# Performance work log

Measured on AMD Instinct MI355X. Metric: run time of the kernel, lower is better.

## Reference

```python
import jax, jax.numpy as jnp
import numpy as np

UNITS = 1024

def setup_inputs() -> dict:
    key = jax.random.key(0)
    k1, k2, k3 = jax.random.split(key, 3)
    B, T, F = 128, 256, 4
    sequence = jax.random.normal(k1, (B, T, F), dtype=jnp.float32)
    # small init scale keeps the ReLU cell state from exploding over 256 steps
    W = jax.random.normal(k2, (F, 4 * UNITS), dtype=jnp.float32) * 0.05
    U = jax.random.normal(k3, (UNITS, 4 * UNITS), dtype=jnp.float32) * 0.02
    b = jnp.zeros((4 * UNITS,), dtype=jnp.float32)
    return {"sequence": sequence, "W": W, "U": U, "b": b}

def _lstm_relu(sequence, W, U, b):
    B = sequence.shape[0]
    h0 = jnp.zeros((B, UNITS), dtype=sequence.dtype)
    c0 = jnp.zeros((B, UNITS), dtype=sequence.dtype)
    # precompute input projections for all timesteps: [T, B, 4H]
    x_proj = jnp.einsum('btf,fg->tbg', sequence, W) + b

    def step(carry, xp_t):
        h, c = carry
        z = xp_t + h @ U  # [B, 4H], gate order i,f,c,o (Keras)
        zi, zf, zg, zo = jnp.split(z, 4, axis=-1)
        i = jax.nn.sigmoid(zi)
        f = jax.nn.sigmoid(zf)
        g = jax.nn.relu(zg)          # activation=relu for candidate
        o = jax.nn.sigmoid(zo)
        c_new = f * c + i * g
        h_new = o * jax.nn.relu(c_new)  # activation=relu on cell output
        return (h_new, c_new), h_new

    (h_last, c_last), outs = jax.lax.scan(step, (h0, c0), x_proj)
    output = jnp.transpose(outs, (1, 0, 2))  # [B, T, H]
    return output, h_last, c_last

def reference(sequence, W, U, b):
    return _lstm_relu(sequence, W, U, b)
```

## Files before the change

### kernel.cpp

```cpp
#include <hip/hip_runtime.h>
#include <hip/hip_bf16.h>
#include <cstdint>


#define B_SZ   128
#define T_SZ   256
#define H_SZ   1024
#define G_SZ   4096

typedef __attribute__((ext_vector_type(8))) short short8;
typedef __attribute__((ext_vector_type(4))) float f32x4;

__device__ __forceinline__ short f2bf(float f) {
    union { float f; unsigned u; } a; a.f = f;
    unsigned r = a.u + 0x7fffu + ((a.u >> 16) & 1u);
    return (short)(r >> 16);
}

__device__ __forceinline__ float sigmoidf_(float x) {
    return 1.0f / (1.0f + __expf(-x));
}

__device__ __forceinline__ short8 pack8(f32x4 a, f32x4 b) {
    union { f32x4 v; unsigned u[4]; } ua, ub; ua.v = a; ub.v = b;
    union { short8 s; unsigned d[4]; } r;
    r.d[0] = __builtin_amdgcn_perm(ua.u[1] + 0x8000u, ua.u[0] + 0x8000u, 0x07060302u);
    r.d[1] = __builtin_amdgcn_perm(ua.u[3] + 0x8000u, ua.u[2] + 0x8000u, 0x07060302u);
    r.d[2] = __builtin_amdgcn_perm(ub.u[1] + 0x8000u, ub.u[0] + 0x8000u, 0x07060302u);
    r.d[3] = __builtin_amdgcn_perm(ub.u[3] + 0x8000u, ub.u[2] + 0x8000u, 0x07060302u);
    return r.s;
}

template<int BF16EX>
__global__ __launch_bounds__(256, 1)
void lstm_persistent(const float* __restrict__ x, const float* __restrict__ W,
                     const float* __restrict__ U, const float* __restrict__ bias,
                     float* __restrict__ out, unsigned* __restrict__ flags,
                     short* __restrict__ ex)
{
    __shared__ __align__(16) char smem[65536];
    short* Ust = (short*)smem;
    float* zpA = (float*)smem;
    float* zpB = (float*)(smem + 32768);

    const int tid  = threadIdx.x;
    const int bid  = blockIdx.x;
    const int rb   = bid >> 6;
    const int jb   = bid & 63;
    const int w    = tid >> 6;
    const int lane = tid & 63;
    const int q    = lane >> 4;
    const int n    = lane & 15;

    short8 bfrag[8][4];
    for (int kc = 0; kc < 4; ++kc) {
        const int kbase = kc * 256;
        for (int i = tid; i < 256 * 64; i += 256) {
            int k = i >> 6, col = i & 63;
            int gcol = (col >> 4) * 1024 + jb * 16 + (col & 15);
            Ust[k * 64 + col] = f2bf(U[(size_t)(kbase + k) * G_SZ + gcol]);
        }
        __syncthreads();
        if (w == kc) {
            #pragma unroll
            for (int kk = 0; kk < 8; ++kk) {
                #pragma unroll
                for (int g = 0; g < 4; ++g) {
                    short8 bb;
                    #pragma unroll
                    for (int jj = 0; jj < 8; ++jj)
                        bb[jj] = Ust[(kk * 32 + q * 8 + jj) * 64 + g * 16 + n];
                    bfrag[kk][g] = bb;
                }
            }
        }
        __syncthreads();
    }

    const int row_l  = tid >> 4;
    const int hid_l  = tid & 15;
    const int hid_g  = jb * 16 + hid_l;
    const int row_g0 = rb * 32 + row_l;
    const int row_g1 = row_g0 + 16;
    const int qr = row_l >> 2, vr = row_l & 3;
    float Wr[4][4], br[4];
    #pragma unroll
    for (int g = 0; g < 4; ++g) {
        br[g] = bias[g * 1024 + hid_g];
        #pragma unroll
        for (int f = 0; f < 4; ++f)
            Wr[g][f] = W[(size_t)f * G_SZ + g * 1024 + hid_g];
    }
    float c0 = 0.f, c1 = 0.f;

    const int arow0 = rb * 32 + n;
    const int krow  = w * 256 + q * 8;
    const unsigned* pollp = flags + rb * 256 + w * 64 + lane;
    unsigned* pubp = flags + rb * 256 + jb * 4 + w;

    for (int t = 0; t < T_SZ; ++t) {
        f32x4 xv0 = *(const f32x4*)(x + ((size_t)row_g0 * T_SZ + t) * 4);
        f32x4 xv1 = *(const f32x4*)(x + ((size_t)row_g1 * T_SZ + t) * 4);

        short8 af[8][2];
        if (t == 0) {
            short8 z = {};
            #pragma unroll
            for (int kk = 0; kk < 8; ++kk) { af[kk][0] = z; af[kk][1] = z; }
        } else {
            for (;;) {
                unsigned v = __hip_atomic_load(pollp, __ATOMIC_RELAXED,
                                               __HIP_MEMORY_SCOPE_AGENT);
                if (__all((int)(v >= (unsigned)t))) break;
                __builtin_amdgcn_s_sleep(2);
            }
            __atomic_signal_fence(__ATOMIC_ACQUIRE);

            if (BF16EX) {
                #pragma unroll
                for (int kk = 0; kk < 8; ++kk) {
                    #pragma unroll
                    for (int mt = 0; mt < 2; ++mt) {
                        const short* p = ex +
                            ((size_t)(arow0 + mt * 16) * T_SZ + (t - 1)) * H_SZ +
                            krow + kk * 32;
                        af[kk][mt] = *(const short8*)p;
                    }
                }
            } else {
                #pragma unroll
                for (int kk = 0; kk < 8; ++kk) {
                    #pragma unroll
                    for (int mt = 0; mt < 2; ++mt) {
                        const float* p = out +
                            ((size_t)(arow0 + mt * 16) * T_SZ + (t - 1)) * H_SZ +
                            krow + kk * 32;
                        f32x4 lo = *(const f32x4*)p;
                        f32x4 hi = *(const f32x4*)(p + 4);
                        af[kk][mt] = pack8(lo, hi);
                    }
                }
            }
        }

        f32x4 acc[2][4];
        #pragma unroll
        for (int mt = 0; mt < 2; ++mt)
            #pragma unroll
            for (int g = 0; g < 4; ++g)
                acc[mt][g] = (f32x4){0.f, 0.f, 0.f, 0.f};

        #pragma unroll
        for (int kk = 0; kk < 8; ++kk)
            #pragma unroll
            for (int mt = 0; mt < 2; ++mt)
                #pragma unroll
                for (int g = 0; g < 4; ++g)
                    acc[mt][g] = __builtin_amdgcn_mfma_f32_16x16x32_bf16(
                        af[kk][mt], bfrag[kk][g], acc[mt][g], 0, 0, 0);

        float* zp = (t & 1) ? zpB : zpA;
        #pragma unroll
        for (int mt = 0; mt < 2; ++mt)
            #pragma unroll
            for (int g = 0; g < 4; ++g)
                *(f32x4*)&zp[(((w * 2 + mt) * 4 + g) * 4 + q) * 64 + n * 4] =
                    acc[mt][g];
        __syncthreads();

        float hn0, hn1;
        {
            float z[4];
            #pragma unroll
            for (int g = 0; g < 4; ++g) {
                float s = br[g];
                #pragma unroll
                for (int ww = 0; ww < 4; ++ww)
                    s += zp[(((ww * 2 + 0) * 4 + g) * 4 + qr) * 64 + hid_l * 4 + vr];
                s += xv0[0] * Wr[g][0] + xv0[1] * Wr[g][1] +
                     xv0[2] * Wr[g][2] + xv0[3] * Wr[g][3];
                z[g] = s;
            }
            float ig = sigmoidf_(z[0]), fg = sigmoidf_(z[1]);
            float gg = fmaxf(z[2], 0.f), og = sigmoidf_(z[3]);
            c0 = fg * c0 + ig * gg;
            hn0 = og * fmaxf(c0, 0.f);
        }
        {
            float z[4];
            #pragma unroll
            for (int g = 0; g < 4; ++g) {
                float s = br[g];
                #pragma unroll
                for (int ww = 0; ww < 4; ++ww)
                    s += zp[(((ww * 2 + 1) * 4 + g) * 4 + qr) * 64 + hid_l * 4 + vr];
                s += xv1[0] * Wr[g][0] + xv1[1] * Wr[g][1] +
                     xv1[2] * Wr[g][2] + xv1[3] * Wr[g][3];
                z[g] = s;
            }
            float ig = sigmoidf_(z[0]), fg = sigmoidf_(z[1]);
            float gg = fmaxf(z[2], 0.f), og = sigmoidf_(z[3]);
            c1 = fg * c1 + ig * gg;
            hn1 = og * fmaxf(c1, 0.f);
        }

        if (BF16EX) {
            float o0 = __shfl_down(hn0, 1);
            float o1 = __shfl_down(hn1, 1);
            if ((hid_l & 1) == 0) {
                unsigned w0 = (unsigned)(unsigned short)f2bf(hn0) |
                              ((unsigned)(unsigned short)f2bf(o0) << 16);
                unsigned w1 = (unsigned)(unsigned short)f2bf(hn1) |
                              ((unsigned)(unsigned short)f2bf(o1) << 16);
                __hip_atomic_store(
                    (unsigned*)&ex[((size_t)row_g0 * T_SZ + t) * H_SZ + hid_g],
                    w0, __ATOMIC_RELAXED, __HIP_MEMORY_SCOPE_AGENT);
                __hip_atomic_store(
                    (unsigned*)&ex[((size_t)row_g1 * T_SZ + t) * H_SZ + hid_g],
                    w1, __ATOMIC_RELAXED, __HIP_MEMORY_SCOPE_AGENT);
            }
            out[((size_t)row_g0 * T_SZ + t) * H_SZ + hid_g] = hn0;
            out[((size_t)row_g1 * T_SZ + t) * H_SZ + hid_g] = hn1;
        } else {
            __hip_atomic_store((unsigned*)&out[((size_t)row_g0 * T_SZ + t) * H_SZ + hid_g],
                               __float_as_uint(hn0), __ATOMIC_RELAXED,
                               __HIP_MEMORY_SCOPE_AGENT);
            __hip_atomic_store((unsigned*)&out[((size_t)row_g1 * T_SZ + t) * H_SZ + hid_g],
                               __float_as_uint(hn1), __ATOMIC_RELAXED,
                               __HIP_MEMORY_SCOPE_AGENT);
        }

        if (t == T_SZ - 1) {
            float* hlast = out + (size_t)B_SZ * T_SZ * H_SZ;
            float* clast = hlast + (size_t)B_SZ * H_SZ;
            hlast[(size_t)row_g0 * H_SZ + hid_g] = hn0;
            hlast[(size_t)row_g1 * H_SZ + hid_g] = hn1;
            clast[(size_t)row_g0 * H_SZ + hid_g] = c0;
            clast[(size_t)row_g1 * H_SZ + hid_g] = c1;
        } else {
            asm volatile("s_waitcnt vmcnt(0)" ::: "memory");
            if (lane == 0)
                __hip_atomic_store(pubp, (unsigned)(t + 1),
                                   __ATOMIC_RELAXED, __HIP_MEMORY_SCOPE_AGENT);
        }
    }
}

extern "C" void kernel_launch(void* const* d_in, const int* in_sizes, int n_in,
                              void* d_out, int out_size, void* d_ws, size_t ws_size,
                              hipStream_t stream) {
    const float* x    = (const float*)d_in[0];
    const float* W    = (const float*)d_in[1];
    const float* U    = (const float*)d_in[2];
    const float* bias = (const float*)d_in[3];
    float* out = (float*)d_out;

    unsigned* flags = (unsigned*)d_ws;
    short* ex = (short*)((char*)d_ws + 4096);

    hipMemsetAsync(d_ws, 0, 4096, stream);

    const size_t need = 4096 + (size_t)B_SZ * T_SZ * H_SZ * sizeof(short);
    if (ws_size >= need) {
        hipLaunchKernelGGL((lstm_persistent<1>), dim3(256), dim3(256), 0, stream,
                           x, W, U, bias, out, flags, ex);
    } else {
        hipLaunchKernelGGL((lstm_persistent<0>), dim3(256), dim3(256), 0, stream,
                           x, W, U, bias, out, flags, ex);
    }
}
```

Baseline: 1.645 ms.

## Retile persistent LSTM blocks to 16 rows by 32 hidden units

Reassigns each persistent block from 32 batch rows × 16 hidden units to 16 batch rows × 32 hidden units. Each block now holds twice the U fragments in registers, and each sync group shrinks from 64 to 32 producers per row cluster. Padded LDS strides are added to reduce bank conflicts. The fp32 output store is moved after the flag publish so the BF16 exchange no longer waits on it. The cost is higher register pressure from 64 B fragments and a different polling pattern, which could spill or lower clocks.

```diff
diff --git a/kernel.cpp b/kernel.cpp
--- a/kernel.cpp
+++ b/kernel.cpp
@@ -7,9 +7,12 @@
 #define T_SZ   256
 #define H_SZ   1024
 #define G_SZ   4096
+#define ULD    130
+#define ZLD    68
 
 typedef __attribute__((ext_vector_type(8))) short short8;
 typedef __attribute__((ext_vector_type(4))) float f32x4;
+typedef __attribute__((ext_vector_type(2))) float f32x2;
 
 __device__ __forceinline__ short f2bf(float f) {
     union { float f; unsigned u; } a; a.f = f;
@@ -38,75 +41,78 @@
                      float* __restrict__ out, unsigned* __restrict__ flags,
                      short* __restrict__ ex)
 {
-    __shared__ __align__(16) char smem[65536];
+    __shared__ __align__(16) char smem[69632];
     short* Ust = (short*)smem;
     float* zpA = (float*)smem;
-    float* zpB = (float*)(smem + 32768);
+    float* zpB = (float*)(smem + 34816);
 
     const int tid  = threadIdx.x;
     const int bid  = blockIdx.x;
-    const int rb   = bid >> 6;
-    const int jb   = bid & 63;
+    const int cl   = bid & 7;
+    const int jbb  = bid >> 3;
     const int w    = tid >> 6;
     const int lane = tid & 63;
     const int q    = lane >> 4;
     const int n    = lane & 15;
 
-    short8 bfrag[8][4];
+    short8 bfrag[8][8];
     for (int kc = 0; kc < 4; ++kc) {
         const int kbase = kc * 256;
-        for (int i = tid; i < 256 * 64; i += 256) {
-            int k = i >> 6, col = i & 63;
-            int gcol = (col >> 4) * 1024 + jb * 16 + (col & 15);
-            Ust[k * 64 + col] = f2bf(U[(size_t)(kbase + k) * G_SZ + gcol]);
+        for (int i = tid; i < 256 * 128; i += 256) {
+            int k = i >> 7, col = i & 127;
+            int g = col >> 5, rem = col & 31;
+            Ust[k * ULD + col] =
+                f2bf(U[(size_t)(kbase + k) * G_SZ + g * 1024 + jbb * 32 + rem]);
         }
         __syncthreads();
         if (w == kc) {
             #pragma unroll
             for (int kk = 0; kk < 8; ++kk) {
                 #pragma unroll
-                for (int g = 0; g < 4; ++g) {
+                for (int tile = 0; tile < 8; ++tile) {
                     short8 bb;
                     #pragma unroll
                     for (int jj = 0; jj < 8; ++jj)
-                        bb[jj] = Ust[(kk * 32 + q * 8 + jj) * 64 + g * 16 + n];
-                    bfrag[kk][g] = bb;
+                        bb[jj] = Ust[(kk * 32 + q * 8 + jj) * ULD + tile * 16 + n];
+                    bfrag[kk][tile] = bb;
                 }
             }
         }
         __syncthreads();
     }
 
-    const int row_l  = tid >> 4;
-    const int hid_l  = tid & 15;
-    const int hid_g  = jb * 16 + hid_l;
-    const int row_g0 = rb * 32 + row_l;
-    const int row_g1 = row_g0 + 16;
-    const int qr = row_l >> 2, vr = row_l & 3;
-    float Wr[4][4], br[4];
+    const int r_l   = tid >> 4;
+    const int cp    = tid & 15;
+    const int row_g = cl * 16 + r_l;
+    const int u0    = jbb * 32 + cp * 2;
+    const int hf    = cp >> 3;
+    const int c0    = (cp * 2) & 15;
+    const int qr    = r_l >> 2, vr = r_l & 3;
+    float Wr[2][4][4], br[2][4];
     #pragma unroll
-    for (int g = 0; g < 4; ++g) {
-        br[g] = bias[g * 1024 + hid_g];
-        #pragma unroll
-        for (int f = 0; f < 4; ++f)
-            Wr[g][f] = W[(size_t)f * G_SZ + g * 1024 + hid_g];
-    }
-    float c0 = 0.f, c1 = 0.f;
-
-    const int arow0 = rb * 32 + n;
-    const int krow  = w * 256 + q * 8;
-    const unsigned* pollp = flags + rb * 256 + w * 64 + lane;
-    unsigned* pubp = flags + rb * 256 + jb * 4 + w;
+    for (int j = 0; j < 2; ++j)
+        #pragma unroll
+        for (int g = 0; g < 4; ++g) {
+            br[j][g] = bias[g * 1024 + u0 + j];
+            #pragma unroll
+            for (int f = 0; f < 4; ++f)
+                Wr[j][g][f] = W[(size_t)f * G_SZ + g * 1024 + u0 + j];
+        }
+    float cst[2] = {0.f, 0.f};
+
+    const int arow = cl * 16 + n;
+    const int krow = w * 256 + q * 8;
+    const unsigned* pollp = flags + cl * 128 + w * 32 + (lane & 31);
+    unsigned* pubp = flags + cl * 128 + jbb * 4 + w;
 
     for (int t = 0; t < T_SZ; ++t) {
-        f32x4 xv0 = *(const f32x4*)(x + ((size_t)row_g0 * T_SZ + t) * 4);
-        f32x4 xv1 = *(const f32x4*)(x + ((size_t)row_g1 * T_SZ + t) * 4);
-
-        short8 af[8][2];
+        f32x4 xv = *(const f32x4*)(x + ((size_t)row_g * T_SZ + t) * 4);
+
+        short8 af[8];
         if (t == 0) {
             short8 z = {};
             #pragma unroll
-            for (int kk = 0; kk < 8; ++kk) { af[kk][0] = z; af[kk][1] = z; }
+            for (int kk = 0; kk < 8; ++kk) af[kk] = z;
         } else {
             for (;;) {
                 unsigned v = __hip_atomic_load(pollp, __ATOMIC_RELAXED,
@@ -118,130 +124,88 @@
 
             if (BF16EX) {
                 #pragma unroll
+                for (int kk = 0; kk < 8; ++kk)
+                    af[kk] = *(const short8*)(ex +
+                        ((size_t)arow * T_SZ + (t - 1)) * H_SZ + krow + kk * 32);
+            } else {
+                #pragma unroll
                 for (int kk = 0; kk < 8; ++kk) {
-                    #pragma unroll
-                    for (int mt = 0; mt < 2; ++mt) {
-                        const short* p = ex +
-                            ((size_t)(arow0 + mt * 16) * T_SZ + (t - 1)) * H_SZ +
-                            krow + kk * 32;
-                        af[kk][mt] = *(const short8*)p;
-                    }
+                    const float* p = out +
+                        ((size_t)arow * T_SZ + (t - 1)) * H_SZ + krow + kk * 32;
+                    f32x4 lo = *(const f32x4*)p;
+                    f32x4 hi = *(const f32x4*)(p + 4);
+                    af[kk] = pack8(lo, hi);
                 }
-            } else {
-                #pragma unroll
-                for (int kk = 0; kk < 8; ++kk) {
-                    #pragma unroll
-                    for (int mt = 0; mt < 2; ++mt) {
-                        const float* p = out +
-                            ((size_t)(arow0 + mt * 16) * T_SZ + (t - 1)) * H_SZ +
-                            krow + kk * 32;
-                        f32x4 lo = *(const f32x4*)p;
-                        f32x4 hi = *(const f32x4*)(p + 4);
-                        af[kk][mt] = pack8(lo, hi);
-                    }
-                }
-            }
-        }
-
-        f32x4 acc[2][4];
-        #pragma unroll
-        for (int mt = 0; mt < 2; ++mt)
-            #pragma unroll
-            for (int g = 0; g < 4; ++g)
-                acc[mt][g] = (f32x4){0.f, 0.f, 0.f, 0.f};
+            }
+        }
+
+        f32x4 acc[8];
+        #pragma unroll
+        for (int tl = 0; tl < 8; ++tl) acc[tl] = (f32x4){0.f, 0.f, 0.f, 0.f};
 
         #pragma unroll
         for (int kk = 0; kk < 8; ++kk)
             #pragma unroll
-            for (int mt = 0; mt < 2; ++mt)
-                #pragma unroll
-                for (int g = 0; g < 4; ++g)
-                    acc[mt][g] = __builtin_amdgcn_mfma_f32_16x16x32_bf16(
-                        af[kk][mt], bfrag[kk][g], acc[mt][g], 0, 0, 0);
+            for (int tl = 0; tl < 8; ++tl)
+                acc[tl] = __builtin_amdgcn_mfma_f32_16x16x32_bf16(
+                    af[kk], bfrag[kk][tl], acc[tl], 0, 0, 0);
 
         float* zp = (t & 1) ? zpB : zpA;
         #pragma unroll
-        for (int mt = 0; mt < 2; ++mt)
-            #pragma unroll
-            for (int g = 0; g < 4; ++g)
-                *(f32x4*)&zp[(((w * 2 + mt) * 4 + g) * 4 + q) * 64 + n * 4] =
-                    acc[mt][g];
+        for (int tl = 0; tl < 8; ++tl)
+            *(f32x4*)&zp[(size_t)(((w * 8 + tl) * 4 + q) * ZLD) + n * 4] = acc[tl];
         __syncthreads();
 
-        float hn0, hn1;
-        {
+        float hh[2];
+        #pragma unroll
+        for (int j = 0; j < 2; ++j) {
             float z[4];
             #pragma unroll
             for (int g = 0; g < 4; ++g) {
-                float s = br[g];
+                float s = br[j][g];
                 #pragma unroll
                 for (int ww = 0; ww < 4; ++ww)
-                    s += zp[(((ww * 2 + 0) * 4 + g) * 4 + qr) * 64 + hid_l * 4 + vr];
-                s += xv0[0] * Wr[g][0] + xv0[1] * Wr[g][1] +
-                     xv0[2] * Wr[g][2] + xv0[3] * Wr[g][3];
+                    s += zp[(size_t)(((ww * 8 + g * 2 + hf) * 4 + qr) * ZLD) +
+                            (c0 + j) * 4 + vr];
+                s += xv[0] * Wr[j][g][0] + xv[1] * Wr[j][g][1] +
+                     xv[2] * Wr[j][g][2] + xv[3] * Wr[j][g][3];
                 z[g] = s;
             }
             float ig = sigmoidf_(z[0]), fg = sigmoidf_(z[1]);
             float gg = fmaxf(z[2], 0.f), og = sigmoidf_(z[3]);
-            c0 = fg * c0 + ig * gg;
-            hn0 = og * fmaxf(c0, 0.f);
-        }
-        {
-            float z[4];
-            #pragma unroll
-            for (int g = 0; g < 4; ++g) {
-                float s = br[g];
-                #pragma unroll
-                for (int ww = 0; ww < 4; ++ww)
-                    s += zp[(((ww * 2 + 1) * 4 + g) * 4 + qr) * 64 + hid_l * 4 + vr];
-                s += xv1[0] * Wr[g][0] + xv1[1] * Wr[g][1] +
-                     xv1[2] * Wr[g][2] + xv1[3] * Wr[g][3];
-                z[g] = s;
-            }
-            float ig = sigmoidf_(z[0]), fg = sigmoidf_(z[1]);
-            float gg = fmaxf(z[2], 0.f), og = sigmoidf_(z[3]);
-            c1 = fg * c1 + ig * gg;
-            hn1 = og * fmaxf(c1, 0.f);
-        }
-
+            cst[j] = fg * cst[j] + ig * gg;
+            hh[j] = og * fmaxf(cst[j], 0.f);
+        }
+
+        const size_t obase = ((size_t)row_g * T_SZ + t) * H_SZ + u0;
         if (BF16EX) {
-            float o0 = __shfl_down(hn0, 1);
-            float o1 = __shfl_down(hn1, 1);
-            if ((hid_l & 1) == 0) {
-                unsigned w0 = (unsigned)(unsigned short)f2bf(hn0) |
-                              ((unsigned)(unsigned short)f2bf(o0) << 16);
-                unsigned w1 = (unsigned)(unsigned short)f2bf(hn1) |
-                              ((unsigned)(unsigned short)f2bf(o1) << 16);
-                __hip_atomic_store(
-                    (unsigned*)&ex[((size_t)row_g0 * T_SZ + t) * H_SZ + hid_g],
-                    w0, __ATOMIC_RELAXED, __HIP_MEMORY_SCOPE_AGENT);
-                __hip_atomic_store(
-                    (unsigned*)&ex[((size_t)row_g1 * T_SZ + t) * H_SZ + hid_g],
-                    w1, __ATOMIC_RELAXED, __HIP_MEMORY_SCOPE_AGENT);
-            }
-            out[((size_t)row_g0 * T_SZ + t) * H_SZ + hid_g] = hn0;
-            out[((size_t)row_g1 * T_SZ + t) * H_SZ + hid_g] = hn1;
+            unsigned pw = (unsigned)(unsigned short)f2bf(hh[0]) |
+                          ((unsigned)(unsigned short)f2bf(hh[1]) << 16);
+            __hip_atomic_store((unsigned*)&ex[obase], pw, __ATOMIC_RELAXED,
+                               __HIP_MEMORY_SCOPE_AGENT);
         } else {
-            __hip_atomic_store((unsigned*)&out[((size_t)row_g0 * T_SZ + t) * H_SZ + hid_g],
-                               __float_as_uint(hn0), __ATOMIC_RELAXED,
-                               __HIP_MEMORY_SCOPE_AGENT);
-            __hip_atomic_store((unsigned*)&out[((size_t)row_g1 * T_SZ + t) * H_SZ + hid_g],
-                               __float_as_uint(hn1), __ATOMIC_RELAXED,
-                               __HIP_MEMORY_SCOPE_AGENT);
-        }
-
-        if (t == T_SZ - 1) {
-            float* hlast = out + (size_t)B_SZ * T_SZ * H_SZ;
-            float* clast = hlast + (size_t)B_SZ * H_SZ;
-            hlast[(size_t)row_g0 * H_SZ + hid_g] = hn0;
-            hlast[(size_t)row_g1 * H_SZ + hid_g] = hn1;
-            clast[(size_t)row_g0 * H_SZ + hid_g] = c0;
-            clast[(size_t)row_g1 * H_SZ + hid_g] = c1;
-        } else {
+            __hip_atomic_store((unsigned*)&out[obase], __float_as_uint(hh[0]),
+                               __ATOMIC_RELAXED, __HIP_MEMORY_SCOPE_AGENT);
+            __hip_atomic_store((unsigned*)&out[obase + 1], __float_as_uint(hh[1]),
+                               __ATOMIC_RELAXED, __HIP_MEMORY_SCOPE_AGENT);
+        }
+
+        if (t != T_SZ - 1) {
             asm volatile("s_waitcnt vmcnt(0)" ::: "memory");
             if (lane == 0)
                 __hip_atomic_store(pubp, (unsigned)(t + 1),
                                    __ATOMIC_RELAXED, __HIP_MEMORY_SCOPE_AGENT);
+        }
+
+        if (BF16EX) {
+            *(f32x2*)&out[obase] = (f32x2){hh[0], hh[1]};
+        }
+
+        if (t == T_SZ - 1) {
+            float* hlast = out + (size_t)B_SZ * T_SZ * H_SZ;
+            float* clast = hlast + (size_t)B_SZ * H_SZ;
+            *(f32x2*)&hlast[(size_t)row_g * H_SZ + u0] = (f32x2){hh[0], hh[1]};
+            *(f32x2*)&clast[(size_t)row_g * H_SZ + u0] = (f32x2){cst[0], cst[1]};
         }
     }
 }
```

Result: slower. 2.137 ms (+29.9%).
